# Kernel optimization log

Measured on AMD Instinct MI355X. Metric: run time of the kernel, lower is better.

Reference implementation:

```python
import jax, jax.numpy as jnp
import numpy as np

N, E, F_IN, HID, HEADS, L, G = 20000, 200000, 20, 128, 4, 4, 32
NEG_SLOPE = 0.2


def setup_inputs() -> dict:
    key = jax.random.key(0)
    ks = jax.random.split(key, 12)
    s = 0.05
    x = jax.random.normal(ks[0], (N, F_IN), jnp.float32)
    edge_index = jax.random.randint(ks[1], (2, E), 0, N, jnp.int32)
    batch = jnp.sort(jax.random.randint(ks[2], (N,), 0, G, jnp.int32))
    W_in = jax.random.normal(ks[3], (F_IN, HID), jnp.float32) * s
    b_in = jnp.zeros((HID,), jnp.float32)
    gat_W = jax.random.normal(ks[4], (L, HID, HEADS * HID), jnp.float32) * s
    att_src = jax.random.normal(ks[5], (L, HEADS, HID), jnp.float32) * s
    att_dst = jax.random.normal(ks[6], (L, HEADS, HID), jnp.float32) * s
    gat_b = jnp.zeros((L, HID), jnp.float32)
    W1 = jax.random.normal(ks[7], (HID, HID // 2), jnp.float32) * s
    b1 = jnp.zeros((HID // 2,), jnp.float32)
    W2 = jax.random.normal(ks[8], (HID // 2, 64), jnp.float32) * s
    b2 = jnp.zeros((64,), jnp.float32)
    W3 = jax.random.normal(ks[9], (64, 32), jnp.float32) * s
    b3 = jnp.zeros((32,), jnp.float32)
    return dict(x=x, edge_index=edge_index, batch=batch, W_in=W_in, b_in=b_in,
                gat_W=gat_W, att_src=att_src, att_dst=att_dst, gat_b=gat_b,
                W1=W1, b1=b1, W2=W2, b2=b2, W3=W3, b3=b3)


def _gat_layer(x, src, dst, W, a_src, a_dst, b):
    # x: [N, HID]; W: [HID, HEADS*HID]; a_*: [HEADS, HID]
    xl = (x @ W).reshape(N, HEADS, HID)                      # [N, H, C]
    al_src = jnp.einsum('nhc,hc->nh', xl, a_src)             # [N, H]
    al_dst = jnp.einsum('nhc,hc->nh', xl, a_dst)             # [N, H]
    e = jax.nn.leaky_relu(al_src[src] + al_dst[dst], NEG_SLOPE)  # [Etot, H]
    # segment softmax over incoming edges of each dst node
    m = jax.ops.segment_max(e, dst, num_segments=N)          # [N, H]
    e = jnp.exp(e - m[dst])
    z = jax.ops.segment_sum(e, dst, num_segments=N)          # [N, H]
    alpha = e / (z[dst] + 1e-16)                             # [Etot, H]
    msg = xl[src] * alpha[:, :, None]                        # [Etot, H, C]
    out = jax.ops.segment_sum(msg, dst, num_segments=N)      # [N, H, C]
    return out.mean(axis=1) + b                              # concat=False: mean over heads


def reference(x, edge_index, batch, W_in, b_in, gat_W, att_src, att_dst, gat_b,
              W1, b1, W2, b2, W3, b3):
    # add self-loops (PyG GATConv default)
    loops = jnp.arange(N, dtype=edge_index.dtype)
    src = jnp.concatenate([edge_index[0], loops])
    dst = jnp.concatenate([edge_index[1], loops])
    h = jax.nn.relu(x @ W_in + b_in)
    for l in range(L):
        h = jax.nn.relu(_gat_layer(h, src, dst, gat_W[l], att_src[l], att_dst[l], gat_b[l])) + h
    # global mean pool per graph
    sums = jax.ops.segment_sum(h, batch, num_segments=G)     # [G, HID]
    cnt = jax.ops.segment_sum(jnp.ones((N,), h.dtype), batch, num_segments=G)
    g = sums / jnp.maximum(cnt, 1.0)[:, None]
    # output MLP (dropout is identity in eval mode)
    g = jax.nn.relu(g @ W1 + b1)
    g = jax.nn.relu(g @ W2 + b2)
    return g @ W3 + b3                                        # [G, 32]
```

## Files before the change

### kernel.cpp

```cpp
#include <hip/hip_runtime.h>

#define N_NODES 20000
#define N_PAD   20032
#define N_EDGES 200000
#define ETOT    (N_EDGES + N_NODES)
#define F_IN    20
#define HID     128
#define HEADS   4
#define FTOT    (HEADS * HID)
#define LAYERS  4
#define NGRAPH  32
#define NEG_SLOPE 0.2f
#define DEG_CAP 64

typedef __attribute__((ext_vector_type(8))) unsigned short ushortx8;
typedef __attribute__((ext_vector_type(8))) short short8;
typedef __attribute__((ext_vector_type(4))) float f32x4;

static __device__ __forceinline__ unsigned short f2bf(float f) {
    unsigned u = __float_as_uint(f);
    u += 0x7FFFu + ((u >> 16) & 1u);
    return (unsigned short)(u >> 16);
}
static __device__ __forceinline__ float bf2f(unsigned short s) {
    return __uint_as_float(((unsigned)s) << 16);
}


__global__ void k_hist(const int* __restrict__ ei, int* __restrict__ deg) {
    int i = blockIdx.x * blockDim.x + threadIdx.x;
    if (i >= ETOT) return;
    int d = (i < N_EDGES) ? ei[N_EDGES + i] : (i - N_EDGES);
    atomicAdd(&deg[d], 1);
}

__global__ __launch_bounds__(1024) void k_scan(const int* __restrict__ deg, int* __restrict__ off) {
    __shared__ int wsum[16];
    __shared__ int carry_s;
    int tid  = threadIdx.x;
    int lane = tid & 63, wv = tid >> 6;
    if (tid == 0) carry_s = 0;
    __syncthreads();
    for (int base = 0; base < N_NODES; base += 1024) {
        int idx = base + tid;
        int v = (idx < N_NODES) ? deg[idx] : 0;
        int x = v;
        #pragma unroll
        for (int s = 1; s < 64; s <<= 1) {
            int t = __shfl_up(x, s, 64);
            if (lane >= s) x += t;
        }
        if (lane == 63) wsum[wv] = x;
        __syncthreads();
        if (wv == 0) {
            int ws = (lane < 16) ? wsum[lane] : 0;
            #pragma unroll
            for (int s = 1; s < 16; s <<= 1) {
                int t = __shfl_up(ws, s, 64);
                if (lane >= s) ws += t;
            }
            if (lane < 16) wsum[lane] = ws;
        }
        __syncthreads();
        int wprev = (wv == 0) ? 0 : wsum[wv - 1];
        int incl  = carry_s + wprev + x;
        if (idx < N_NODES) off[idx] = incl - v;
        __syncthreads();
        if (tid == 1023) carry_s = incl;
        __syncthreads();
    }
    if (threadIdx.x == 0) off[N_NODES] = carry_s;
}

__global__ void k_scatter(const int* __restrict__ ei, const int* __restrict__ off,
                          int* __restrict__ cur, int* __restrict__ csr_src) {
    int i = blockIdx.x * blockDim.x + threadIdx.x;
    if (i >= ETOT) return;
    int s, d;
    if (i < N_EDGES) { s = ei[i]; d = ei[N_EDGES + i]; }
    else             { s = d = i - N_EDGES; }
    int pos = off[d] + atomicAdd(&cur[d], 1);
    csr_src[pos] = s;
}


__global__ void k_bounds(const int* __restrict__ batch, int* __restrict__ gstart) {
    int i = blockIdx.x * blockDim.x + threadIdx.x;
    if (i >= N_NODES) return;
    int b = batch[i];
    int prev = (i == 0) ? -1 : batch[i - 1];
    for (int g = prev + 1; g <= b; ++g) gstart[g] = i;
    if (i == N_NODES - 1) {
        for (int g = b + 1; g <= NGRAPH; ++g) gstart[g] = N_NODES;
    }
}


__global__ void k_wconv(const float* __restrict__ W, unsigned short* __restrict__ wswz) {
    int o = blockIdx.x * 256 + threadIdx.x;
    if (o >= LAYERS * 32 * 4 * 64 * 8) return;
    int e    = o & 7;
    int lane = (o >> 3) & 63;
    int kc   = (o >> 9) & 3;
    int cg   = (o >> 11) & 31;
    int l    = o >> 16;
    int k    = kc * 32 + (lane >> 4) * 8 + e;
    int col  = cg * 16 + (lane & 15);
    wswz[o] = f2bf(W[((size_t)l * HID + k) * FTOT + col]);
}


__global__ __launch_bounds__(256) void k_inproj(const float* __restrict__ x,
                                                const float* __restrict__ W,
                                                const float* __restrict__ b,
                                                float* __restrict__ h,
                                                unsigned short* __restrict__ hb) {
    __shared__ float xs[2][F_IN];
    int tid = threadIdx.x;
    int node0 = blockIdx.x * 2;
    if (tid < 2 * F_IN) {
        int r = tid / F_IN, k = tid % F_IN;
        int nd = node0 + r;
        xs[r][k] = (nd < N_NODES) ? x[nd * F_IN + k] : 0.f;
    }
    __syncthreads();
    int ln = tid >> 7;
    int c  = tid & 127;
    int node = node0 + ln;
    if (node >= N_NODES) return;
    float s = b[c];
    #pragma unroll
    for (int k = 0; k < F_IN; ++k) s += xs[ln][k] * W[k * HID + c];
    float r = fmaxf(s, 0.f);
    h[(size_t)node * HID + c] = r;
    hb[(size_t)node * HID + c] = f2bf(r);
}


__global__ __launch_bounds__(256) void k_gemm(const unsigned short* __restrict__ hb,
                                              const unsigned short* __restrict__ wswz,
                                              const float* __restrict__ asrc,
                                              const float* __restrict__ adst,
                                              unsigned short* __restrict__ xl,
                                              float* __restrict__ al_s,
                                              float* __restrict__ al_d) {
    int tid  = threadIdx.x;
    int lane = tid & 63;
    int w    = tid >> 6;
    int r0   = blockIdx.x * 64 + w * 16;
    int hd   = blockIdx.y;
    int arow = r0 + (lane & 15);
    const short8* ap = (const short8*)(hb + (size_t)arow * HID + (lane >> 4) * 8);
    const short8* bp = (const short8*)wswz;
    short8 a[4];
    #pragma unroll
    for (int kc = 0; kc < 4; ++kc) a[kc] = ap[kc * 4];
    f32x4 acc[8];
    #pragma unroll
    for (int ct = 0; ct < 8; ++ct) {
        f32x4 c = {0.f, 0.f, 0.f, 0.f};
        int cg = hd * 8 + ct;
        #pragma unroll
        for (int kc = 0; kc < 4; ++kc) {
            short8 b = bp[(cg * 4 + kc) * 64 + lane];
            c = __builtin_amdgcn_mfma_f32_16x16x32_bf16(a[kc], b, c, 0, 0, 0);
        }
        acc[ct] = c;
    }
    int ocol = lane & 15;
    int orow = r0 + (lane >> 4) * 4;
    float vs[4] = {}, vd[4] = {};
    #pragma unroll
    for (int ct = 0; ct < 8; ++ct) {
        int colg = hd * 128 + ct * 16 + ocol;
        float as = asrc[colg], ad = adst[colg];
        #pragma unroll
        for (int r = 0; r < 4; ++r) {
            vs[r] += acc[ct][r] * as;
            vd[r] += acc[ct][r] * ad;
            int row = orow + r;
            if (row < N_NODES) xl[(size_t)row * FTOT + colg] = f2bf(acc[ct][r]);
        }
    }
    #pragma unroll
    for (int msk = 1; msk < 16; msk <<= 1) {
        #pragma unroll
        for (int r = 0; r < 4; ++r) {
            vs[r] += __shfl_xor(vs[r], msk, 64);
            vd[r] += __shfl_xor(vd[r], msk, 64);
        }
    }
    if (ocol == 0) {
        #pragma unroll
        for (int r = 0; r < 4; ++r) {
            int row = orow + r;
            if (row < N_NODES) {
                al_s[row * HEADS + hd] = vs[r];
                al_d[row * HEADS + hd] = vd[r];
            }
        }
    }
}


__global__ __launch_bounds__(256) void k_agg(const unsigned short* __restrict__ xl,
                                             const float* __restrict__ al_s,
                                             const float* __restrict__ al_d,
                                             const int* __restrict__ csr_off,
                                             const int* __restrict__ csr_src,
                                             const float* __restrict__ bias,
                                             float* __restrict__ h,
                                             unsigned short* __restrict__ hb) {
    __shared__ float alds[4][DEG_CAP][HEADS];
    int tid  = threadIdx.x;
    int lane = tid & 63;
    int wid  = tid >> 6;
    int node = blockIdx.x * 4 + wid;
    if (node >= N_NODES) return;
    int hh = lane >> 4;
    int el = lane & 15;
    int e0 = csr_off[node], e1 = csr_off[node + 1];
    int deg = e1 - e0;
    float ald = al_d[node * HEADS + hh];

    float ev0 = -1e30f, ev1 = -1e30f, ev2 = -1e30f, ev3 = -1e30f;
    {
        if (el < deg) {
            int s = csr_src[e0 + el];
            float e = al_s[s * HEADS + hh] + ald;
            ev0 = e > 0.f ? e : NEG_SLOPE * e;
        }
        if (el + 16 < deg) {
            int s = csr_src[e0 + el + 16];
            float e = al_s[s * HEADS + hh] + ald;
            ev1 = e > 0.f ? e : NEG_SLOPE * e;
        }
        if (el + 32 < deg) {
            int s = csr_src[e0 + el + 32];
            float e = al_s[s * HEADS + hh] + ald;
            ev2 = e > 0.f ? e : NEG_SLOPE * e;
        }
        if (el + 48 < deg) {
            int s = csr_src[e0 + el + 48];
            float e = al_s[s * HEADS + hh] + ald;
            ev3 = e > 0.f ? e : NEG_SLOPE * e;
        }
    }
    float m = fmaxf(fmaxf(ev0, ev1), fmaxf(ev2, ev3));
    float z = 0.f;
    if (el      < deg) z += __expf(ev0 - m);
    if (el + 16 < deg) z += __expf(ev1 - m);
    if (el + 32 < deg) z += __expf(ev2 - m);
    if (el + 48 < deg) z += __expf(ev3 - m);
    for (int i = el + DEG_CAP; i < deg; i += 16) {
        int s = csr_src[e0 + i];
        float e = al_s[s * HEADS + hh] + ald;
        e = e > 0.f ? e : NEG_SLOPE * e;
        float mn = fmaxf(m, e);
        z = z * __expf(m - mn) + __expf(e - mn);
        m = mn;
    }
    #pragma unroll
    for (int msk = 1; msk < 16; msk <<= 1) {
        float m2 = __shfl_xor(m, msk, 64);
        float z2 = __shfl_xor(z, msk, 64);
        float mn = fmaxf(m, m2);
        z = z * __expf(m - mn) + z2 * __expf(m2 - mn);
        m = mn;
    }
    float zinv = 1.f / (z + 1e-16f);
    if (el      < deg) alds[wid][el     ][hh] = __expf(ev0 - m);
    if (el + 16 < deg) alds[wid][el + 16][hh] = __expf(ev1 - m);
    if (el + 32 < deg) alds[wid][el + 32][hh] = __expf(ev2 - m);
    if (el + 48 < deg) alds[wid][el + 48][hh] = __expf(ev3 - m);
    __syncthreads();

    float acc[8] = {};
    const unsigned short* xbase = xl + lane * 8;
    int dcap = deg < DEG_CAP ? deg : DEG_CAP;
    int i = 0;
    for (; i + 1 < dcap; i += 2) {
        int s0 = csr_src[e0 + i];
        int s1 = csr_src[e0 + i + 1];
        float a0 = alds[wid][i][hh];
        float a1 = alds[wid][i + 1][hh];
        ushortx8 v0 = *(const ushortx8*)(xbase + (size_t)s0 * FTOT);
        ushortx8 v1 = *(const ushortx8*)(xbase + (size_t)s1 * FTOT);
        #pragma unroll
        for (int j = 0; j < 8; ++j) acc[j] += a0 * bf2f(v0[j]) + a1 * bf2f(v1[j]);
    }
    if (i < dcap) {
        int s0 = csr_src[e0 + i];
        float a0 = alds[wid][i][hh];
        ushortx8 v0 = *(const ushortx8*)(xbase + (size_t)s0 * FTOT);
        #pragma unroll
        for (int j = 0; j < 8; ++j) acc[j] += a0 * bf2f(v0[j]);
    }
    for (int t = DEG_CAP; t < deg; ++t) {
        int s0 = csr_src[e0 + t];
        float e = al_s[s0 * HEADS + hh] + ald;
        e = e > 0.f ? e : NEG_SLOPE * e;
        float a0 = __expf(e - m);
        ushortx8 v0 = *(const ushortx8*)(xbase + (size_t)s0 * FTOT);
        #pragma unroll
        for (int j = 0; j < 8; ++j) acc[j] += a0 * bf2f(v0[j]);
    }
    #pragma unroll
    for (int j = 0; j < 8; ++j) {
        acc[j] *= zinv;
        acc[j] += __shfl_xor(acc[j], 16, 64);
        acc[j] += __shfl_xor(acc[j], 32, 64);
    }
    if (lane < 16) {
        int c = lane * 8;
        float4 hv0 = *(const float4*)(h + (size_t)node * HID + c);
        float4 hv1 = *(const float4*)(h + (size_t)node * HID + c + 4);
        float4 b0 = *(const float4*)(bias + c);
        float4 b1 = *(const float4*)(bias + c + 4);
        float o0 = fmaxf(acc[0] * 0.25f + b0.x, 0.f) + hv0.x;
        float o1 = fmaxf(acc[1] * 0.25f + b0.y, 0.f) + hv0.y;
        float o2 = fmaxf(acc[2] * 0.25f + b0.z, 0.f) + hv0.z;
        float o3 = fmaxf(acc[3] * 0.25f + b0.w, 0.f) + hv0.w;
        float o4 = fmaxf(acc[4] * 0.25f + b1.x, 0.f) + hv1.x;
        float o5 = fmaxf(acc[5] * 0.25f + b1.y, 0.f) + hv1.y;
        float o6 = fmaxf(acc[6] * 0.25f + b1.z, 0.f) + hv1.z;
        float o7 = fmaxf(acc[7] * 0.25f + b1.w, 0.f) + hv1.w;
        *(float4*)(h + (size_t)node * HID + c)     = make_float4(o0, o1, o2, o3);
        *(float4*)(h + (size_t)node * HID + c + 4) = make_float4(o4, o5, o6, o7);
        ushortx8 hv;
        hv[0] = f2bf(o0); hv[1] = f2bf(o1); hv[2] = f2bf(o2); hv[3] = f2bf(o3);
        hv[4] = f2bf(o4); hv[5] = f2bf(o5); hv[6] = f2bf(o6); hv[7] = f2bf(o7);
        *(ushortx8*)(hb + (size_t)node * HID + c) = hv;
    }
}


__global__ __launch_bounds__(128) void k_pool(const float* __restrict__ h,
                                              const int* __restrict__ gstart,
                                              float* __restrict__ pooled) {
    int g = blockIdx.y;
    int slice = blockIdx.x;
    int tid = threadIdx.x;
    int start = gstart[g];
    int cnt   = gstart[g + 1] - start;
    int per = (cnt + 31) / 32;
    int r0 = slice * per, r1 = min(r0 + per, cnt);
    if (r0 >= r1) return;
    float s0 = 0.f, s1 = 0.f, s2 = 0.f, s3 = 0.f;
    int r = r0;
    for (; r + 3 < r1; r += 4) {
        s0 += h[(size_t)(start + r)     * HID + tid];
        s1 += h[(size_t)(start + r + 1) * HID + tid];
        s2 += h[(size_t)(start + r + 2) * HID + tid];
        s3 += h[(size_t)(start + r + 3) * HID + tid];
    }
    for (; r < r1; ++r) s0 += h[(size_t)(start + r) * HID + tid];
    atomicAdd(&pooled[g * HID + tid], (s0 + s1) + (s2 + s3));
}

__global__ __launch_bounds__(256) void k_mlp(const float* __restrict__ pooled,
                                             const int* __restrict__ gstart,
                                             const float* __restrict__ W1, const float* __restrict__ b1,
                                             const float* __restrict__ W2, const float* __restrict__ b2,
                                             const float* __restrict__ W3, const float* __restrict__ b3,
                                             float* __restrict__ out) {
    int gr = blockIdx.x;
    __shared__ float g[HID];
    __shared__ float part[4][64];
    __shared__ float t1[64], t2[64];
    int tid = threadIdx.x;
    if (tid < HID) {
        float inv = 1.f / fmaxf((float)(gstart[gr + 1] - gstart[gr]), 1.f);
        g[tid] = pooled[gr * HID + tid] * inv;
    }
    __syncthreads();
    {
        int c = tid & 63, q = tid >> 6;
        float s = 0.f;
        #pragma unroll 8
        for (int k = q * 32; k < q * 32 + 32; ++k) s += g[k] * W1[k * 64 + c];
        part[q][c] = s;
        __syncthreads();
        if (tid < 64) t1[tid] = fmaxf(part[0][tid] + part[1][tid] + part[2][tid] + part[3][tid] + b1[tid], 0.f);
        __syncthreads();
    }
    {
        int c = tid & 63, q = tid >> 6;
        float s = 0.f;
        #pragma unroll 8
        for (int k = q * 16; k < q * 16 + 16; ++k) s += t1[k] * W2[k * 64 + c];
        part[q][c] = s;
        __syncthreads();
        if (tid < 64) t2[tid] = fmaxf(part[0][tid] + part[1][tid] + part[2][tid] + part[3][tid] + b2[tid], 0.f);
        __syncthreads();
    }
    {
        int c = tid & 31, q = tid >> 5;
        float s = 0.f;
        #pragma unroll 8
        for (int k = q * 8; k < q * 8 + 8; ++k) s += t2[k] * W3[k * 32 + c];
        float* pf = &part[0][0];
        pf[q * 32 + c] = s;
        __syncthreads();
        if (tid < 32) {
            float r = b3[tid];
            #pragma unroll
            for (int q2 = 0; q2 < 8; ++q2) r += pf[q2 * 32 + tid];
            out[gr * 32 + tid] = r;
        }
    }
}


extern "C" void kernel_launch(void* const* d_in, const int* in_sizes, int n_in,
                              void* d_out, int out_size, void* d_ws, size_t ws_size,
                              hipStream_t stream) {
    const float* x       = (const float*)d_in[0];
    const int*   ei      = (const int*)d_in[1];
    const int*   batch   = (const int*)d_in[2];
    const float* W_in    = (const float*)d_in[3];
    const float* b_in    = (const float*)d_in[4];
    const float* gat_W   = (const float*)d_in[5];
    const float* att_src = (const float*)d_in[6];
    const float* att_dst = (const float*)d_in[7];
    const float* gat_b   = (const float*)d_in[8];
    const float* W1 = (const float*)d_in[9];
    const float* b1 = (const float*)d_in[10];
    const float* W2 = (const float*)d_in[11];
    const float* b2 = (const float*)d_in[12];
    const float* W3 = (const float*)d_in[13];
    const float* b3 = (const float*)d_in[14];
    float* out = (float*)d_out;

    char* ws = (char*)d_ws;
    size_t o = 0;
    auto alloc = [&](size_t nbytes) -> void* {
        void* p = ws + o;
        o += (nbytes + 255) & ~(size_t)255;
        return p;
    };
    int* deg      = (int*)alloc((size_t)2 * N_NODES * 4);
    int* cur      = deg + N_NODES;
    int* gstart   = (int*)alloc((size_t)(NGRAPH + 1) * 4);
    float* pooled = (float*)alloc((size_t)NGRAPH * HID * 4);
    int* csr_off  = (int*)alloc((size_t)(N_NODES + 1) * 4);
    int* csr_src  = (int*)alloc((size_t)ETOT * 4);
    float* h      = (float*)alloc((size_t)N_NODES * HID * 4);
    unsigned short* hb   = (unsigned short*)alloc((size_t)N_PAD * HID * 2);
    unsigned short* xl   = (unsigned short*)alloc((size_t)N_NODES * FTOT * 2);
    unsigned short* wswz = (unsigned short*)alloc((size_t)LAYERS * HID * FTOT * 2);
    float* al_s   = (float*)alloc((size_t)N_NODES * HEADS * 4);
    float* al_d   = (float*)alloc((size_t)N_NODES * HEADS * 4);

    hipMemsetAsync(deg, 0, (size_t)2 * N_NODES * 4, stream);
    hipMemsetAsync(pooled, 0, (size_t)NGRAPH * HID * 4, stream);

    k_hist<<<(ETOT + 255) / 256, 256, 0, stream>>>(ei, deg);
    k_scan<<<1, 1024, 0, stream>>>(deg, csr_off);
    k_scatter<<<(ETOT + 255) / 256, 256, 0, stream>>>(ei, csr_off, cur, csr_src);
    k_bounds<<<(N_NODES + 255) / 256, 256, 0, stream>>>(batch, gstart);
    k_wconv<<<(LAYERS * 32 * 4 * 64 * 8) / 256, 256, 0, stream>>>(gat_W, wswz);

    k_inproj<<<(N_NODES + 1) / 2, 256, 0, stream>>>(x, W_in, b_in, h, hb);

    for (int l = 0; l < LAYERS; ++l) {
        k_gemm<<<dim3(N_PAD / 64, HEADS), 256, 0, stream>>>(
            hb, wswz + (size_t)l * HID * FTOT,
            att_src + (size_t)l * HEADS * HID, att_dst + (size_t)l * HEADS * HID,
            xl, al_s, al_d);
        k_agg<<<(N_NODES + 3) / 4, 256, 0, stream>>>(
            xl, al_s, al_d, csr_off, csr_src, gat_b + (size_t)l * HID, h, hb);
    }

    k_pool<<<dim3(32, NGRAPH), 128, 0, stream>>>(h, gstart, pooled);
    k_mlp<<<NGRAPH, 256, 0, stream>>>(pooled, gstart, W1, b1, W2, b2, W3, b3, out);
}
```

Measured before the change: 366.5 us.

## Aggregate raw features before projection and precompute W·a attention vectors

Reorders each GAT layer so attention logits come from h times precomputed W·a vectors, and neighbour aggregation runs over 128-wide h rows per head instead of 512-wide projected rows. The per-head aggregates are then multiplied by a reshaped weight (K=512, N=128) in a new MFMA GEMM that also applies bias, mean over heads, ReLU and the residual. This is meant to shrink gather traffic per edge and drop the large xl write and read. The cost is a larger K in the GEMM, an extra uagg buffer, and a rounding order that differs from the reference. It also merges the batch-bounds kernel into the histogram kernel and combines the two memsets.

```diff
diff --git a/kernel.cpp b/kernel.cpp
--- a/kernel.cpp
+++ b/kernel.cpp
@@ -27,11 +27,21 @@
 }
 
 
-__global__ void k_hist(const int* __restrict__ ei, int* __restrict__ deg) {
+__global__ void k_histb(const int* __restrict__ ei, const int* __restrict__ batch,
+                        int* __restrict__ deg, int* __restrict__ gstart) {
     int i = blockIdx.x * blockDim.x + threadIdx.x;
-    if (i >= ETOT) return;
-    int d = (i < N_EDGES) ? ei[N_EDGES + i] : (i - N_EDGES);
-    atomicAdd(&deg[d], 1);
+    if (i < ETOT) {
+        int d = (i < N_EDGES) ? ei[N_EDGES + i] : (i - N_EDGES);
+        atomicAdd(&deg[d], 1);
+    }
+    if (i < N_NODES) {
+        int b = batch[i];
+        int prev = (i == 0) ? -1 : batch[i - 1];
+        for (int g = prev + 1; g <= b; ++g) gstart[g] = i;
+        if (i == N_NODES - 1) {
+            for (int g = b + 1; g <= NGRAPH; ++g) gstart[g] = N_NODES;
+        }
+    }
 }
 
 __global__ __launch_bounds__(1024) void k_scan(const int* __restrict__ deg, int* __restrict__ off) {
@@ -84,29 +94,35 @@
 }
 
 
-__global__ void k_bounds(const int* __restrict__ batch, int* __restrict__ gstart) {
-    int i = blockIdx.x * blockDim.x + threadIdx.x;
-    if (i >= N_NODES) return;
-    int b = batch[i];
-    int prev = (i == 0) ? -1 : batch[i - 1];
-    for (int g = prev + 1; g <= b; ++g) gstart[g] = i;
-    if (i == N_NODES - 1) {
-        for (int g = b + 1; g <= NGRAPH; ++g) gstart[g] = N_NODES;
-    }
-}
-
-
 __global__ void k_wconv(const float* __restrict__ W, unsigned short* __restrict__ wswz) {
     int o = blockIdx.x * 256 + threadIdx.x;
-    if (o >= LAYERS * 32 * 4 * 64 * 8) return;
+    if (o >= LAYERS * 8 * 16 * 64 * 8) return;
     int e    = o & 7;
     int lane = (o >> 3) & 63;
-    int kc   = (o >> 9) & 3;
-    int cg   = (o >> 11) & 31;
+    int kc   = (o >> 9) & 15;
+    int cg   = (o >> 13) & 7;
     int l    = o >> 16;
-    int k    = kc * 32 + (lane >> 4) * 8 + e;
-    int col  = cg * 16 + (lane & 15);
-    wswz[o] = f2bf(W[((size_t)l * HID + k) * FTOT + col]);
+    int ks   = kc * 32 + (lane >> 4) * 8 + e;
+    int c    = cg * 16 + (lane & 15);
+    int j    = ks & 127, hd = ks >> 7;
+    wswz[o] = f2bf(W[((size_t)l * HID + j) * FTOT + hd * HID + c]);
+}
+
+
+__global__ void k_wa(const float* __restrict__ W, const float* __restrict__ asrc,
+                     const float* __restrict__ adst, float* __restrict__ wa) {
+    int t = blockIdx.x * 256 + threadIdx.x;
+    if (t >= LAYERS * 2 * HEADS * HID) return;
+    int j  = t & 127;
+    int h  = (t >> 7) & 3;
+    int sd = (t >> 9) & 1;
+    int l  = t >> 10;
+    const float* a    = (sd ? adst : asrc) + ((size_t)l * HEADS + h) * HID;
+    const float* Wrow = W + ((size_t)l * HID + j) * FTOT + h * HID;
+    float s = 0.f;
+    #pragma unroll 4
+    for (int c = 0; c < HID; ++c) s += Wrow[c] * a[c];
+    wa[t] = s;
 }
 
 
@@ -137,86 +153,45 @@
 }
 
 
-__global__ __launch_bounds__(256) void k_gemm(const unsigned short* __restrict__ hb,
-                                              const unsigned short* __restrict__ wswz,
-                                              const float* __restrict__ asrc,
-                                              const float* __restrict__ adst,
-                                              unsigned short* __restrict__ xl,
-                                              float* __restrict__ al_s,
-                                              float* __restrict__ al_d) {
-    int tid  = threadIdx.x;
-    int lane = tid & 63;
-    int w    = tid >> 6;
-    int r0   = blockIdx.x * 64 + w * 16;
-    int hd   = blockIdx.y;
-    int arow = r0 + (lane & 15);
-    const short8* ap = (const short8*)(hb + (size_t)arow * HID + (lane >> 4) * 8);
-    const short8* bp = (const short8*)wswz;
-    short8 a[4];
+__global__ __launch_bounds__(256) void k_att(const unsigned short* __restrict__ hb,
+                                             const float* __restrict__ wa,
+                                             float* __restrict__ al_s,
+                                             float* __restrict__ al_d) {
+    __shared__ float wl[2 * HEADS * HID];
+    int tid = threadIdx.x;
+    for (int i = tid; i < 2 * HEADS * HID; i += 256) wl[i] = wa[i];
+    __syncthreads();
+    int nl = tid >> 3;
+    int h  = tid & 3;
+    int sd = (tid >> 2) & 1;
+    int node = blockIdx.x * 32 + nl;
+    const unsigned short* row = hb + (size_t)node * HID;
+    const float* w = wl + (sd * HEADS + h) * HID;
+    float s = 0.f;
     #pragma unroll
-    for (int kc = 0; kc < 4; ++kc) a[kc] = ap[kc * 4];
-    f32x4 acc[8];
-    #pragma unroll
-    for (int ct = 0; ct < 8; ++ct) {
-        f32x4 c = {0.f, 0.f, 0.f, 0.f};
-        int cg = hd * 8 + ct;
+    for (int j0 = 0; j0 < HID; j0 += 8) {
+        ushortx8 v = *(const ushortx8*)(row + j0);
         #pragma unroll
-        for (int kc = 0; kc < 4; ++kc) {
-            short8 b = bp[(cg * 4 + kc) * 64 + lane];
-            c = __builtin_amdgcn_mfma_f32_16x16x32_bf16(a[kc], b, c, 0, 0, 0);
-        }
-        acc[ct] = c;
-    }
-    int ocol = lane & 15;
-    int orow = r0 + (lane >> 4) * 4;
-    float vs[4] = {}, vd[4] = {};
-    #pragma unroll
-    for (int ct = 0; ct < 8; ++ct) {
-        int colg = hd * 128 + ct * 16 + ocol;
-        float as = asrc[colg], ad = adst[colg];
-        #pragma unroll
-        for (int r = 0; r < 4; ++r) {
-            vs[r] += acc[ct][r] * as;
-            vd[r] += acc[ct][r] * ad;
-            int row = orow + r;
-            if (row < N_NODES) xl[(size_t)row * FTOT + colg] = f2bf(acc[ct][r]);
-        }
-    }
-    #pragma unroll
-    for (int msk = 1; msk < 16; msk <<= 1) {
-        #pragma unroll
-        for (int r = 0; r < 4; ++r) {
-            vs[r] += __shfl_xor(vs[r], msk, 64);
-            vd[r] += __shfl_xor(vd[r], msk, 64);
-        }
-    }
-    if (ocol == 0) {
-        #pragma unroll
-        for (int r = 0; r < 4; ++r) {
-            int row = orow + r;
-            if (row < N_NODES) {
-                al_s[row * HEADS + hd] = vs[r];
-                al_d[row * HEADS + hd] = vd[r];
-            }
-        }
-    }
-}
-
-
-__global__ __launch_bounds__(256) void k_agg(const unsigned short* __restrict__ xl,
+        for (int e = 0; e < 8; ++e) s += bf2f(v[e]) * w[j0 + e];
+    }
+    if (sd == 0) al_s[node * HEADS + h] = s;
+    else         al_d[node * HEADS + h] = s;
+}
+
+
+__global__ __launch_bounds__(256) void k_agg(const unsigned short* __restrict__ hb,
                                              const float* __restrict__ al_s,
                                              const float* __restrict__ al_d,
                                              const int* __restrict__ csr_off,
                                              const int* __restrict__ csr_src,
-                                             const float* __restrict__ bias,
-                                             float* __restrict__ h,
-                                             unsigned short* __restrict__ hb) {
+                                             unsigned short* __restrict__ u) {
     __shared__ float alds[4][DEG_CAP][HEADS];
+    __shared__ float zlds[4][HEADS];
+    __shared__ float mlds[4][HEADS];
     int tid  = threadIdx.x;
     int lane = tid & 63;
     int wid  = tid >> 6;
     int node = blockIdx.x * 4 + wid;
-    if (node >= N_NODES) return;
     int hh = lane >> 4;
     int el = lane & 15;
     int e0 = csr_off[node], e1 = csr_off[node + 1];
@@ -224,27 +199,25 @@
     float ald = al_d[node * HEADS + hh];
 
     float ev0 = -1e30f, ev1 = -1e30f, ev2 = -1e30f, ev3 = -1e30f;
-    {
-        if (el < deg) {
-            int s = csr_src[e0 + el];
-            float e = al_s[s * HEADS + hh] + ald;
-            ev0 = e > 0.f ? e : NEG_SLOPE * e;
-        }
-        if (el + 16 < deg) {
-            int s = csr_src[e0 + el + 16];
-            float e = al_s[s * HEADS + hh] + ald;
-            ev1 = e > 0.f ? e : NEG_SLOPE * e;
-        }
-        if (el + 32 < deg) {
-            int s = csr_src[e0 + el + 32];
-            float e = al_s[s * HEADS + hh] + ald;
-            ev2 = e > 0.f ? e : NEG_SLOPE * e;
-        }
-        if (el + 48 < deg) {
-            int s = csr_src[e0 + el + 48];
-            float e = al_s[s * HEADS + hh] + ald;
-            ev3 = e > 0.f ? e : NEG_SLOPE * e;
-        }
+    if (el < deg) {
+        int s = csr_src[e0 + el];
+        float e = al_s[s * HEADS + hh] + ald;
+        ev0 = e > 0.f ? e : NEG_SLOPE * e;
+    }
+    if (el + 16 < deg) {
+        int s = csr_src[e0 + el + 16];
+        float e = al_s[s * HEADS + hh] + ald;
+        ev1 = e > 0.f ? e : NEG_SLOPE * e;
+    }
+    if (el + 32 < deg) {
+        int s = csr_src[e0 + el + 32];
+        float e = al_s[s * HEADS + hh] + ald;
+        ev2 = e > 0.f ? e : NEG_SLOPE * e;
+    }
+    if (el + 48 < deg) {
+        int s = csr_src[e0 + el + 48];
+        float e = al_s[s * HEADS + hh] + ald;
+        ev3 = e > 0.f ? e : NEG_SLOPE * e;
     }
     float m = fmaxf(fmaxf(ev0, ev1), fmaxf(ev2, ev3));
     float z = 0.f;
@@ -268,69 +241,122 @@
         z = z * __expf(m - mn) + z2 * __expf(m2 - mn);
         m = mn;
     }
-    float zinv = 1.f / (z + 1e-16f);
+    if (el == 0) {
+        zlds[wid][hh] = 1.f / (z + 1e-16f);
+        mlds[wid][hh] = m;
+    }
     if (el      < deg) alds[wid][el     ][hh] = __expf(ev0 - m);
     if (el + 16 < deg) alds[wid][el + 16][hh] = __expf(ev1 - m);
     if (el + 32 < deg) alds[wid][el + 32][hh] = __expf(ev2 - m);
     if (el + 48 < deg) alds[wid][el + 48][hh] = __expf(ev3 - m);
     __syncthreads();
 
-    float acc[8] = {};
-    const unsigned short* xbase = xl + lane * 8;
+    float a0c0 = 0.f, a1c0 = 0.f, a2c0 = 0.f, a3c0 = 0.f;
+    float a0c1 = 0.f, a1c1 = 0.f, a2c1 = 0.f, a3c1 = 0.f;
+    const unsigned short* xbase = hb + lane * 2;
     int dcap = deg < DEG_CAP ? deg : DEG_CAP;
     int i = 0;
     for (; i + 1 < dcap; i += 2) {
         int s0 = csr_src[e0 + i];
         int s1 = csr_src[e0 + i + 1];
-        float a0 = alds[wid][i][hh];
-        float a1 = alds[wid][i + 1][hh];
-        ushortx8 v0 = *(const ushortx8*)(xbase + (size_t)s0 * FTOT);
-        ushortx8 v1 = *(const ushortx8*)(xbase + (size_t)s1 * FTOT);
-        #pragma unroll
-        for (int j = 0; j < 8; ++j) acc[j] += a0 * bf2f(v0[j]) + a1 * bf2f(v1[j]);
+        unsigned w0 = *(const unsigned*)(xbase + (size_t)s0 * HID);
+        unsigned w1 = *(const unsigned*)(xbase + (size_t)s1 * HID);
+        f32x4 p0 = *(const f32x4*)&alds[wid][i][0];
+        f32x4 p1 = *(const f32x4*)&alds[wid][i + 1][0];
+        float c00 = bf2f((unsigned short)w0), c01 = bf2f((unsigned short)(w0 >> 16));
+        float c10 = bf2f((unsigned short)w1), c11 = bf2f((unsigned short)(w1 >> 16));
+        a0c0 += p0[0] * c00 + p1[0] * c10;  a0c1 += p0[0] * c01 + p1[0] * c11;
+        a1c0 += p0[1] * c00 + p1[1] * c10;  a1c1 += p0[1] * c01 + p1[1] * c11;
+        a2c0 += p0[2] * c00 + p1[2] * c10;  a2c1 += p0[2] * c01 + p1[2] * c11;
+        a3c0 += p0[3] * c00 + p1[3] * c10;  a3c1 += p0[3] * c01 + p1[3] * c11;
     }
     if (i < dcap) {
         int s0 = csr_src[e0 + i];
-        float a0 = alds[wid][i][hh];
-        ushortx8 v0 = *(const ushortx8*)(xbase + (size_t)s0 * FTOT);
+        unsigned w0 = *(const unsigned*)(xbase + (size_t)s0 * HID);
+        f32x4 p0 = *(const f32x4*)&alds[wid][i][0];
+        float c00 = bf2f((unsigned short)w0), c01 = bf2f((unsigned short)(w0 >> 16));
+        a0c0 += p0[0] * c00;  a0c1 += p0[0] * c01;
+        a1c0 += p0[1] * c00;  a1c1 += p0[1] * c01;
+        a2c0 += p0[2] * c00;  a2c1 += p0[2] * c01;
+        a3c0 += p0[3] * c00;  a3c1 += p0[3] * c01;
+    }
+    if (deg > DEG_CAP) {
+        f32x4 ald4 = *(const f32x4*)&al_d[node * HEADS];
+        f32x4 m4;
+        m4[0] = mlds[wid][0]; m4[1] = mlds[wid][1];
+        m4[2] = mlds[wid][2]; m4[3] = mlds[wid][3];
+        for (int t = DEG_CAP; t < deg; ++t) {
+            int s0 = csr_src[e0 + t];
+            unsigned w0 = *(const unsigned*)(xbase + (size_t)s0 * HID);
+            float c00 = bf2f((unsigned short)w0), c01 = bf2f((unsigned short)(w0 >> 16));
+            #pragma unroll
+            for (int hd = 0; hd < 4; ++hd) {
+                float e = al_s[s0 * HEADS + hd] + ald4[hd];
+                e = e > 0.f ? e : NEG_SLOPE * e;
+                float p = __expf(e - m4[hd]);
+                if (hd == 0) { a0c0 += p * c00; a0c1 += p * c01; }
+                if (hd == 1) { a1c0 += p * c00; a1c1 += p * c01; }
+                if (hd == 2) { a2c0 += p * c00; a2c1 += p * c01; }
+                if (hd == 3) { a3c0 += p * c00; a3c1 += p * c01; }
+            }
+        }
+    }
+    f32x4 zi = *(const f32x4*)&zlds[wid][0];
+    unsigned short* ubase = u + (size_t)node * FTOT + lane * 2;
+    {
+        unsigned pk0 = (unsigned)f2bf(a0c0 * zi[0]) | ((unsigned)f2bf(a0c1 * zi[0]) << 16);
+        unsigned pk1 = (unsigned)f2bf(a1c0 * zi[1]) | ((unsigned)f2bf(a1c1 * zi[1]) << 16);
+        unsigned pk2 = (unsigned)f2bf(a2c0 * zi[2]) | ((unsigned)f2bf(a2c1 * zi[2]) << 16);
+        unsigned pk3 = (unsigned)f2bf(a3c0 * zi[3]) | ((unsigned)f2bf(a3c1 * zi[3]) << 16);
+        *(unsigned*)(ubase)             = pk0;
+        *(unsigned*)(ubase + HID)       = pk1;
+        *(unsigned*)(ubase + 2 * HID)   = pk2;
+        *(unsigned*)(ubase + 3 * HID)   = pk3;
+    }
+}
+
+
+__global__ __launch_bounds__(256) void k_gemm2(const unsigned short* __restrict__ u,
+                                               const unsigned short* __restrict__ wswz,
+                                               const float* __restrict__ bias,
+                                               float* __restrict__ h,
+                                               unsigned short* __restrict__ hb) {
+    int tid  = threadIdx.x;
+    int lane = tid & 63;
+    int w    = tid >> 6;
+    int r0   = blockIdx.x * 64 + w * 16;
+    int arow = r0 + (lane & 15);
+    const short8* ap = (const short8*)(u + (size_t)arow * FTOT + (lane >> 4) * 8);
+    const short8* bp = (const short8*)wswz;
+    short8 a[16];
+    #pragma unroll
+    for (int kc = 0; kc < 16; ++kc) a[kc] = ap[kc * 4];
+    f32x4 acc[8];
+    #pragma unroll
+    for (int cg = 0; cg < 8; ++cg) {
+        f32x4 c = {0.f, 0.f, 0.f, 0.f};
         #pragma unroll
-        for (int j = 0; j < 8; ++j) acc[j] += a0 * bf2f(v0[j]);
-    }
-    for (int t = DEG_CAP; t < deg; ++t) {
-        int s0 = csr_src[e0 + t];
-        float e = al_s[s0 * HEADS + hh] + ald;
-        e = e > 0.f ? e : NEG_SLOPE * e;
-        float a0 = __expf(e - m);
-        ushortx8 v0 = *(const ushortx8*)(xbase + (size_t)s0 * FTOT);
+        for (int kc = 0; kc < 16; ++kc) {
+            c = __builtin_amdgcn_mfma_f32_16x16x32_bf16(a[kc], bp[(cg * 16 + kc) * 64 + lane], c, 0, 0, 0);
+        }
+        acc[cg] = c;
+    }
+    int ocol = lane & 15;
+    int orow = r0 + (lane >> 4) * 4;
+    #pragma unroll
+    for (int cg = 0; cg < 8; ++cg) {
+        int col = cg * 16 + ocol;
+        float bv = bias[col];
         #pragma unroll
-        for (int j = 0; j < 8; ++j) acc[j] += a0 * bf2f(v0[j]);
-    }
-    #pragma unroll
-    for (int j = 0; j < 8; ++j) {
-        acc[j] *= zinv;
-        acc[j] += __shfl_xor(acc[j], 16, 64);
-        acc[j] += __shfl_xor(acc[j], 32, 64);
-    }
-    if (lane < 16) {
-        int c = lane * 8;
-        float4 hv0 = *(const float4*)(h + (size_t)node * HID + c);
-        float4 hv1 = *(const float4*)(h + (size_t)node * HID + c + 4);
-        float4 b0 = *(const float4*)(bias + c);
-        float4 b1 = *(const float4*)(bias + c + 4);
-        float o0 = fmaxf(acc[0] * 0.25f + b0.x, 0.f) + hv0.x;
-        float o1 = fmaxf(acc[1] * 0.25f + b0.y, 0.f) + hv0.y;
-        float o2 = fmaxf(acc[2] * 0.25f + b0.z, 0.f) + hv0.z;
-        float o3 = fmaxf(acc[3] * 0.25f + b0.w, 0.f) + hv0.w;
-        float o4 = fmaxf(acc[4] * 0.25f + b1.x, 0.f) + hv1.x;
-        float o5 = fmaxf(acc[5] * 0.25f + b1.y, 0.f) + hv1.y;
-        float o6 = fmaxf(acc[6] * 0.25f + b1.z, 0.f) + hv1.z;
-        float o7 = fmaxf(acc[7] * 0.25f + b1.w, 0.f) + hv1.w;
-        *(float4*)(h + (size_t)node * HID + c)     = make_float4(o0, o1, o2, o3);
-        *(float4*)(h + (size_t)node * HID + c + 4) = make_float4(o4, o5, o6, o7);
-        ushortx8 hv;
-        hv[0] = f2bf(o0); hv[1] = f2bf(o1); hv[2] = f2bf(o2); hv[3] = f2bf(o3);
-        hv[4] = f2bf(o4); hv[5] = f2bf(o5); hv[6] = f2bf(o6); hv[7] = f2bf(o7);
-        *(ushortx8*)(hb + (size_t)node * HID + c) = hv;
+        for (int r = 0; r < 4; ++r) {
+            int row = orow + r;
+            if (row < N_NODES) {
+                size_t idx = (size_t)row * HID + col;
+                float val = fmaxf(acc[cg][r] * 0.25f + bv, 0.f) + h[idx];
+                h[idx] = val;
+                hb[idx] = f2bf(val);
+            }
+        }
     }
 }
 
@@ -439,37 +465,38 @@
         o += (nbytes + 255) & ~(size_t)255;
         return p;
     };
-    int* deg      = (int*)alloc((size_t)2 * N_NODES * 4);
+    int* zero_rgn = (int*)alloc((size_t)(2 * N_NODES + NGRAPH * HID) * 4);
+    int* deg      = zero_rgn;
     int* cur      = deg + N_NODES;
+    float* pooled = (float*)(cur + N_NODES);
     int* gstart   = (int*)alloc((size_t)(NGRAPH + 1) * 4);
-    float* pooled = (float*)alloc((size_t)NGRAPH * HID * 4);
     int* csr_off  = (int*)alloc((size_t)(N_NODES + 1) * 4);
     int* csr_src  = (int*)alloc((size_t)ETOT * 4);
     float* h      = (float*)alloc((size_t)N_NODES * HID * 4);
     unsigned short* hb   = (unsigned short*)alloc((size_t)N_PAD * HID * 2);
-    unsigned short* xl   = (unsigned short*)alloc((size_t)N_NODES * FTOT * 2);
-    unsigned short* wswz = (unsigned short*)alloc((size_t)LAYERS * HID * FTOT * 2);
+    unsigned short* uagg = (unsigned short*)alloc((size_t)N_PAD * FTOT * 2);
+    unsigned short* wswz = (unsigned short*)alloc((size_t)LAYERS * FTOT * HID * 2);
+    float* wa     = (float*)alloc((size_t)LAYERS * 2 * HEADS * HID * 4);
     float* al_s   = (float*)alloc((size_t)N_NODES * HEADS * 4);
     float* al_d   = (float*)alloc((size_t)N_NODES * HEADS * 4);
 
-    hipMemsetAsync(deg, 0, (size_t)2 * N_NODES * 4, stream);
-    hipMemsetAsync(pooled, 0, (size_t)NGRAPH * HID * 4, stream);
-
-    k_hist<<<(ETOT + 255) / 256, 256, 0, stream>>>(ei, deg);
+    hipMemsetAsync(zero_rgn, 0, (size_t)(2 * N_NODES + NGRAPH * HID) * 4, stream);
+
+    k_histb<<<(ETOT + 255) / 256, 256, 0, stream>>>(ei, batch, deg, gstart);
     k_scan<<<1, 1024, 0, stream>>>(deg, csr_off);
     k_scatter<<<(ETOT + 255) / 256, 256, 0, stream>>>(ei, csr_off, cur, csr_src);
-    k_bounds<<<(N_NODES + 255) / 256, 256, 0, stream>>>(batch, gstart);
-    k_wconv<<<(LAYERS * 32 * 4 * 64 * 8) / 256, 256, 0, stream>>>(gat_W, wswz);
+    k_wconv<<<(LAYERS * 8 * 16 * 64 * 8) / 256, 256, 0, stream>>>(gat_W, wswz);
+    k_wa<<<(LAYERS * 2 * HEADS * HID + 255) / 256, 256, 0, stream>>>(gat_W, att_src, att_dst, wa);
 
     k_inproj<<<(N_NODES + 1) / 2, 256, 0, stream>>>(x, W_in, b_in, h, hb);
 
     for (int l = 0; l < LAYERS; ++l) {
-        k_gemm<<<dim3(N_PAD / 64, HEADS), 256, 0, stream>>>(
-            hb, wswz + (size_t)l * HID * FTOT,
-            att_src + (size_t)l * HEADS * HID, att_dst + (size_t)l * HEADS * HID,
-            xl, al_s, al_d);
-        k_agg<<<(N_NODES + 3) / 4, 256, 0, stream>>>(
-            xl, al_s, al_d, csr_off, csr_src, gat_b + (size_t)l * HID, h, hb);
+        k_att<<<N_NODES / 32, 256, 0, stream>>>(
+            hb, wa + (size_t)l * 2 * HEADS * HID, al_s, al_d);
+        k_agg<<<N_NODES / 4, 256, 0, stream>>>(
+            hb, al_s, al_d, csr_off, csr_src, uagg);
+        k_gemm2<<<N_PAD / 64, 256, 0, stream>>>(
+            uagg, wswz + (size_t)l * FTOT * HID, gat_b + (size_t)l * HID, h, hb);
     }
 
     k_pool<<<dim3(32, NGRAPH), 128, 0, stream>>>(h, gstart, pooled);
```

New measurement: 396.1 us. +8.1%, slower.

## Split each node's edge aggregation across two wavefronts in k_agg

Applied to the files above, without the earlier changes.

Aggregation now uses 512-thread blocks with two wavefronts per destination node. The first computes the softmax statistics into shared memory, then both gather alternating edges, and their partial sums are combined through shared memory before the epilogue. The aim is to double memory-level parallelism on the latency-bound gather of source features for average-degree nodes. In exchange it adds a second block barrier and shared-memory traffic, and it leaves half the wavefronts idle during the softmax phase. The high-degree tail is still handled by one wavefront only.

```diff
diff --git a/kernel.cpp b/kernel.cpp
--- a/kernel.cpp
+++ b/kernel.cpp
@@ -203,7 +203,7 @@
 }
 
 
-__global__ __launch_bounds__(256) void k_agg(const unsigned short* __restrict__ xl,
+__global__ __launch_bounds__(512) void k_agg(const unsigned short* __restrict__ xl,
                                              const float* __restrict__ al_s,
                                              const float* __restrict__ al_d,
                                              const int* __restrict__ csr_off,
@@ -212,19 +212,23 @@
                                              float* __restrict__ h,
                                              unsigned short* __restrict__ hb) {
     __shared__ float alds[4][DEG_CAP][HEADS];
+    __shared__ float zin[4][HEADS];
+    __shared__ float psum[4][HID];
     int tid  = threadIdx.x;
     int lane = tid & 63;
     int wid  = tid >> 6;
-    int node = blockIdx.x * 4 + wid;
-    if (node >= N_NODES) return;
+    int nip  = wid >> 1;
+    int half = wid & 1;
+    int node = blockIdx.x * 4 + nip;
     int hh = lane >> 4;
     int el = lane & 15;
     int e0 = csr_off[node], e1 = csr_off[node + 1];
     int deg = e1 - e0;
-    float ald = al_d[node * HEADS + hh];
-
-    float ev0 = -1e30f, ev1 = -1e30f, ev2 = -1e30f, ev3 = -1e30f;
-    {
+    float m_keep = -1e30f;
+
+    if (half == 0) {
+        float ald = al_d[node * HEADS + hh];
+        float ev0 = -1e30f, ev1 = -1e30f, ev2 = -1e30f, ev3 = -1e30f;
         if (el < deg) {
             int s = csr_src[e0 + el];
             float e = al_s[s * HEADS + hh] + ald;
@@ -245,45 +249,46 @@
             float e = al_s[s * HEADS + hh] + ald;
             ev3 = e > 0.f ? e : NEG_SLOPE * e;
         }
-    }
-    float m = fmaxf(fmaxf(ev0, ev1), fmaxf(ev2, ev3));
-    float z = 0.f;
-    if (el      < deg) z += __expf(ev0 - m);
-    if (el + 16 < deg) z += __expf(ev1 - m);
-    if (el + 32 < deg) z += __expf(ev2 - m);
-    if (el + 48 < deg) z += __expf(ev3 - m);
-    for (int i = el + DEG_CAP; i < deg; i += 16) {
-        int s = csr_src[e0 + i];
-        float e = al_s[s * HEADS + hh] + ald;
-        e = e > 0.f ? e : NEG_SLOPE * e;
-        float mn = fmaxf(m, e);
-        z = z * __expf(m - mn) + __expf(e - mn);
-        m = mn;
-    }
-    #pragma unroll
-    for (int msk = 1; msk < 16; msk <<= 1) {
-        float m2 = __shfl_xor(m, msk, 64);
-        float z2 = __shfl_xor(z, msk, 64);
-        float mn = fmaxf(m, m2);
-        z = z * __expf(m - mn) + z2 * __expf(m2 - mn);
-        m = mn;
-    }
-    float zinv = 1.f / (z + 1e-16f);
-    if (el      < deg) alds[wid][el     ][hh] = __expf(ev0 - m);
-    if (el + 16 < deg) alds[wid][el + 16][hh] = __expf(ev1 - m);
-    if (el + 32 < deg) alds[wid][el + 32][hh] = __expf(ev2 - m);
-    if (el + 48 < deg) alds[wid][el + 48][hh] = __expf(ev3 - m);
+        float m = fmaxf(fmaxf(ev0, ev1), fmaxf(ev2, ev3));
+        float z = 0.f;
+        if (el      < deg) z += __expf(ev0 - m);
+        if (el + 16 < deg) z += __expf(ev1 - m);
+        if (el + 32 < deg) z += __expf(ev2 - m);
+        if (el + 48 < deg) z += __expf(ev3 - m);
+        for (int i = el + DEG_CAP; i < deg; i += 16) {
+            int s = csr_src[e0 + i];
+            float e = al_s[s * HEADS + hh] + ald;
+            e = e > 0.f ? e : NEG_SLOPE * e;
+            float mn = fmaxf(m, e);
+            z = z * __expf(m - mn) + __expf(e - mn);
+            m = mn;
+        }
+        #pragma unroll
+        for (int msk = 1; msk < 16; msk <<= 1) {
+            float m2 = __shfl_xor(m, msk, 64);
+            float z2 = __shfl_xor(z, msk, 64);
+            float mn = fmaxf(m, m2);
+            z = z * __expf(m - mn) + z2 * __expf(m2 - mn);
+            m = mn;
+        }
+        if (el == 0) zin[nip][hh] = 1.f / (z + 1e-16f);
+        if (el      < deg) alds[nip][el     ][hh] = __expf(ev0 - m);
+        if (el + 16 < deg) alds[nip][el + 16][hh] = __expf(ev1 - m);
+        if (el + 32 < deg) alds[nip][el + 32][hh] = __expf(ev2 - m);
+        if (el + 48 < deg) alds[nip][el + 48][hh] = __expf(ev3 - m);
+        m_keep = m;
+    }
     __syncthreads();
 
     float acc[8] = {};
     const unsigned short* xbase = xl + lane * 8;
     int dcap = deg < DEG_CAP ? deg : DEG_CAP;
-    int i = 0;
-    for (; i + 1 < dcap; i += 2) {
+    int i = half;
+    for (; i + 2 < dcap; i += 4) {
         int s0 = csr_src[e0 + i];
-        int s1 = csr_src[e0 + i + 1];
-        float a0 = alds[wid][i][hh];
-        float a1 = alds[wid][i + 1][hh];
+        int s1 = csr_src[e0 + i + 2];
+        float a0 = alds[nip][i][hh];
+        float a1 = alds[nip][i + 2][hh];
         ushortx8 v0 = *(const ushortx8*)(xbase + (size_t)s0 * FTOT);
         ushortx8 v1 = *(const ushortx8*)(xbase + (size_t)s1 * FTOT);
         #pragma unroll
@@ -291,40 +296,54 @@
     }
     if (i < dcap) {
         int s0 = csr_src[e0 + i];
-        float a0 = alds[wid][i][hh];
+        float a0 = alds[nip][i][hh];
         ushortx8 v0 = *(const ushortx8*)(xbase + (size_t)s0 * FTOT);
         #pragma unroll
         for (int j = 0; j < 8; ++j) acc[j] += a0 * bf2f(v0[j]);
     }
-    for (int t = DEG_CAP; t < deg; ++t) {
-        int s0 = csr_src[e0 + t];
-        float e = al_s[s0 * HEADS + hh] + ald;
-        e = e > 0.f ? e : NEG_SLOPE * e;
-        float a0 = __expf(e - m);
-        ushortx8 v0 = *(const ushortx8*)(xbase + (size_t)s0 * FTOT);
-        #pragma unroll
-        for (int j = 0; j < 8; ++j) acc[j] += a0 * bf2f(v0[j]);
-    }
+    if (half == 0) {
+        float ald = al_d[node * HEADS + hh];
+        for (int t = DEG_CAP; t < deg; ++t) {
+            int s0 = csr_src[e0 + t];
+            float e = al_s[s0 * HEADS + hh] + ald;
+            e = e > 0.f ? e : NEG_SLOPE * e;
+            float a0 = __expf(e - m_keep);
+            ushortx8 v0 = *(const ushortx8*)(xbase + (size_t)s0 * FTOT);
+            #pragma unroll
+            for (int j = 0; j < 8; ++j) acc[j] += a0 * bf2f(v0[j]);
+        }
+    }
+    float zv = zin[nip][hh];
     #pragma unroll
     for (int j = 0; j < 8; ++j) {
-        acc[j] *= zinv;
+        acc[j] *= zv;
         acc[j] += __shfl_xor(acc[j], 16, 64);
         acc[j] += __shfl_xor(acc[j], 32, 64);
     }
-    if (lane < 16) {
+    if (half == 1 && lane < 16) {
         int c = lane * 8;
+        float4 p0 = make_float4(acc[0], acc[1], acc[2], acc[3]);
+        float4 p1 = make_float4(acc[4], acc[5], acc[6], acc[7]);
+        *(float4*)&psum[nip][c]     = p0;
+        *(float4*)&psum[nip][c + 4] = p1;
+    }
+    __syncthreads();
+    if (half == 0 && lane < 16) {
+        int c = lane * 8;
+        float4 q0 = *(const float4*)&psum[nip][c];
+        float4 q1 = *(const float4*)&psum[nip][c + 4];
         float4 hv0 = *(const float4*)(h + (size_t)node * HID + c);
         float4 hv1 = *(const float4*)(h + (size_t)node * HID + c + 4);
         float4 b0 = *(const float4*)(bias + c);
         float4 b1 = *(const float4*)(bias + c + 4);
-        float o0 = fmaxf(acc[0] * 0.25f + b0.x, 0.f) + hv0.x;
-        float o1 = fmaxf(acc[1] * 0.25f + b0.y, 0.f) + hv0.y;
-        float o2 = fmaxf(acc[2] * 0.25f + b0.z, 0.f) + hv0.z;
-        float o3 = fmaxf(acc[3] * 0.25f + b0.w, 0.f) + hv0.w;
-        float o4 = fmaxf(acc[4] * 0.25f + b1.x, 0.f) + hv1.x;
-        float o5 = fmaxf(acc[5] * 0.25f + b1.y, 0.f) + hv1.y;
-        float o6 = fmaxf(acc[6] * 0.25f + b1.z, 0.f) + hv1.z;
-        float o7 = fmaxf(acc[7] * 0.25f + b1.w, 0.f) + hv1.w;
+        float o0 = fmaxf((acc[0] + q0.x) * 0.25f + b0.x, 0.f) + hv0.x;
+        float o1 = fmaxf((acc[1] + q0.y) * 0.25f + b0.y, 0.f) + hv0.y;
+        float o2 = fmaxf((acc[2] + q0.z) * 0.25f + b0.z, 0.f) + hv0.z;
+        float o3 = fmaxf((acc[3] + q0.w) * 0.25f + b0.w, 0.f) + hv0.w;
+        float o4 = fmaxf((acc[4] + q1.x) * 0.25f + b1.x, 0.f) + hv1.x;
+        float o5 = fmaxf((acc[5] + q1.y) * 0.25f + b1.y, 0.f) + hv1.y;
+        float o6 = fmaxf((acc[6] + q1.z) * 0.25f + b1.z, 0.f) + hv1.z;
+        float o7 = fmaxf((acc[7] + q1.w) * 0.25f + b1.w, 0.f) + hv1.w;
         *(float4*)(h + (size_t)node * HID + c)     = make_float4(o0, o1, o2, o3);
         *(float4*)(h + (size_t)node * HID + c + 4) = make_float4(o4, o5, o6, o7);
         ushortx8 hv;
@@ -468,7 +487,7 @@
             hb, wswz + (size_t)l * HID * FTOT,
             att_src + (size_t)l * HEADS * HID, att_dst + (size_t)l * HEADS * HID,
             xl, al_s, al_d);
-        k_agg<<<(N_NODES + 3) / 4, 256, 0, stream>>>(
+        k_agg<<<N_NODES / 4, 512, 0, stream>>>(
             xl, al_s, al_d, csr_off, csr_src, gat_b + (size_t)l * HID, h, hb);
     }
 
```

Result: slower. 384.6 us (+4.9%).
